# Kernel optimization log

Hardware: AMD Instinct MI355X
Metric: run time of the kernel (lower is better)

Reference implementation:

```python
import jax, jax.numpy as jnp
import numpy as np

HID = 128
OUT = 1
L = 4
N_NODES = 50000
N_EDGES = 600000
NUM_GRAPHS = 256
ATOM_FEATS, ATOM_VOCAB = 9, 64
BOND_FEATS, BOND_VOCAB = 3, 8
BN_EPS = 1e-5


def setup_inputs() -> dict:
    key = jax.random.key(0)
    ks = jax.random.split(key, 16)
    x = jax.random.randint(ks[0], (N_NODES, ATOM_FEATS), 0, ATOM_VOCAB)
    edge_index = jax.random.randint(ks[1], (2, N_EDGES), 0, N_NODES)
    edge_attr = jax.random.randint(ks[2], (N_EDGES, BOND_FEATS), 0, BOND_VOCAB)
    batch = jnp.sort(jax.random.randint(ks[3], (N_NODES,), 0, NUM_GRAPHS))
    s = 0.05
    atom_emb = jax.random.normal(ks[4], (ATOM_FEATS, ATOM_VOCAB, HID), jnp.float32) * s
    bond_emb = jax.random.normal(ks[5], (BOND_FEATS, BOND_VOCAB, HID), jnp.float32) * s
    lin1_w = jax.random.normal(ks[6], (L, HID, HID), jnp.float32) * (1.0 / np.sqrt(HID))
    lin1_b = jnp.zeros((L, HID), jnp.float32)
    lin2_w = jax.random.normal(ks[7], (L, HID, HID), jnp.float32) * (1.0 / np.sqrt(HID))
    lin2_b = jnp.zeros((L, HID), jnp.float32)
    bn_gamma = jnp.ones((L, HID), jnp.float32)
    bn_beta = jnp.zeros((L, HID), jnp.float32)
    bn_mean = jax.random.normal(ks[8], (L, HID), jnp.float32) * 0.1
    bn_var = jax.random.uniform(ks[9], (L, HID), jnp.float32, 0.5, 1.5)
    mlp_w = jax.random.normal(ks[10], (HID, OUT), jnp.float32) * (1.0 / np.sqrt(HID))
    mlp_b = jnp.zeros((OUT,), jnp.float32)
    return dict(x=x, edge_index=edge_index, edge_attr=edge_attr, batch=batch,
                atom_emb=atom_emb, bond_emb=bond_emb,
                lin1_w=lin1_w, lin1_b=lin1_b, lin2_w=lin2_w, lin2_b=lin2_b,
                bn_gamma=bn_gamma, bn_beta=bn_beta, bn_mean=bn_mean, bn_var=bn_var,
                mlp_w=mlp_w, mlp_b=mlp_b)


def _multi_embed(tables, idx):
    # tables: [F, V, H], idx: [N, F] -> sum over F of tables[f][idx[:, f]] -> [N, H]
    return jax.vmap(lambda tab, i: tab[i], in_axes=(0, 1))(tables, idx).sum(0)


def reference(x, edge_index, edge_attr, batch, atom_emb, bond_emb,
              lin1_w, lin1_b, lin2_w, lin2_b, bn_gamma, bn_beta,
              bn_mean, bn_var, mlp_w, mlp_b):
    h = _multi_embed(atom_emb, x)            # [N, H]
    e = _multi_embed(bond_emb, edge_attr)    # [E, H]
    src, dst = edge_index[0], edge_index[1]
    for l in range(L):
        x_res = h
        # GINEConv (eps=0): MLP(x + sum_j ReLU(x_j + e_ji))
        msg = jax.nn.relu(h[src] + e)                          # [E, H]
        agg = jax.ops.segment_sum(msg, dst, num_segments=N_NODES)
        z = h + agg
        z = jax.nn.relu(z @ lin1_w[l] + lin1_b[l]) @ lin2_w[l] + lin2_b[l]
        # BatchNorm (eval: running stats)
        z = (z - bn_mean[l]) * (bn_gamma[l] / jnp.sqrt(bn_var[l] + BN_EPS)) + bn_beta[l]
        h = x_res + jax.nn.relu(z)
        # dropout is identity in eval mode
    sums = jax.ops.segment_sum(h, batch, num_segments=NUM_GRAPHS)
    cnt = jax.ops.segment_sum(jnp.ones((N_NODES, 1), h.dtype), batch, num_segments=NUM_GRAPHS)
    pooled = sums / jnp.maximum(cnt, 1.0)
    return pooled @ mlp_w + mlp_b
```

## Files before the change

### kernel.cpp

```cpp
#include <hip/hip_runtime.h>

#define NNODES 50000
#define NEDGES 600000
#define NGRAPH 256
#define HD     128
#define NLAYER 4
#define NBLK_SCAN 49

typedef __bf16 bf16;
typedef __attribute__((ext_vector_type(2))) __bf16 bf16x2;
typedef __attribute__((ext_vector_type(4))) __bf16 bf16x4;
typedef __attribute__((ext_vector_type(8))) __bf16 bf16x8;
typedef __attribute__((ext_vector_type(4))) float  f32x4;

#define CB_MLPW 0
#define CB_MLPB 128

struct PtrPack { const void* p[12]; };

__device__ __forceinline__ float ldf(const void* p, int i, int flag) {
    return flag ? (float)((const bf16*)p)[i] : ((const float*)p)[i];
}
__device__ __forceinline__ float blo(unsigned u) { return __uint_as_float(u << 16); }
__device__ __forceinline__ float bhi(unsigned u) { return __uint_as_float(u & 0xFFFF0000u); }

__global__ __launch_bounds__(256) void k_prep(PtrPack pk, const int* __restrict__ x,
                                              float* __restrict__ cvt, bf16* __restrict__ wtg,
                                              float* __restrict__ biasf, float* __restrict__ scalef,
                                              float* __restrict__ shiftf, bf16* __restrict__ etab,
                                              bf16* __restrict__ hbuf) {
    const int flag = (((const unsigned*)pk.p[6])[0] != 0x3F800000u);
    int b = blockIdx.x, t = threadIdx.x;
    if (b < 512) {
        int idx = b * 256 + t;
        int mat = idx >> 14, rem = idx & 16383;
        int k = rem >> 7, n = rem & 127;
        const void* src = (mat < 4) ? pk.p[2] : pk.p[4];
        int mi = (mat < 4) ? mat : mat - 4;
        wtg[((size_t)mat << 14) + (n << 7) + k] = (bf16)ldf(src, (mi << 14) + (k << 7) + n, flag);
    } else if (b < 514) {
        int i = (b - 512) * 256 + t;
        biasf[i] = ldf(pk.p[3], i, flag);
        float s = ldf(pk.p[6], i, flag) * rsqrtf(ldf(pk.p[9], i, flag) + 1e-5f);
        scalef[i] = s;
        shiftf[i] = (ldf(pk.p[5], i, flag) - ldf(pk.p[8], i, flag)) * s + ldf(pk.p[7], i, flag);
    } else if (b == 514) {
        if (t < 128)       cvt[CB_MLPW + t] = ldf(pk.p[10], t, flag);
        else if (t == 128) cvt[CB_MLPB] = ldf(pk.p[11], 0, flag);
    } else if (b < 771) {
        int idx = (b - 515) * 256 + t;
        int combo = idx >> 7, ch = idx & 127;
        int c0 = combo & 7, c1 = (combo >> 3) & 7, c2 = combo >> 6;
        float v = ldf(pk.p[1], (c0 << 7) + ch, flag) +
                  ldf(pk.p[1], ((8 + c1) << 7) + ch, flag) +
                  ldf(pk.p[1], ((16 + c2) << 7) + ch, flag);
        etab[idx] = (bf16)v;
    } else {
        int wid = t >> 6, lane = t & 63;
        int n = (b - 771) * 4 + wid;
        if (n >= NNODES) return;
        const int* xr = x + n * 9;
        float ax = 0.f, ay = 0.f;
        if (flag) {
            const char* ae = (const char*)pk.p[0];
#pragma unroll
            for (int f = 0; f < 9; ++f) {
                int v = xr[f];
                unsigned hu = *(const unsigned*)(ae + (((size_t)(f * 64 + v)) << 8) + (lane << 2));
                ax += blo(hu); ay += bhi(hu);
            }
        } else {
            const float* ae = (const float*)pk.p[0];
#pragma unroll
            for (int f = 0; f < 9; ++f) {
                int v = xr[f];
                float2 tv = ((const float2*)(ae + (((size_t)(f * 64 + v)) << 7)))[lane];
                ax += tv.x; ay += tv.y;
            }
        }
        bf16x2 hv; hv[0] = (bf16)ax; hv[1] = (bf16)ay;
        ((bf16x2*)(hbuf + ((size_t)n << 7)))[lane] = hv;
    }
}

__global__ void k_hist(const int* __restrict__ ei, int* __restrict__ deg) {
    int i = blockIdx.x * 256 + threadIdx.x;
    if (i < NEDGES) atomicAdd(&deg[ei[NEDGES + i]], 1);
}

__global__ void k_scan1(const int* __restrict__ deg, int* __restrict__ partials) {
    __shared__ int s[256];
    int t = threadIdx.x, b = blockIdx.x;
    int base = b * 1024 + t * 4;
    int sum = 0;
#pragma unroll
    for (int i = 0; i < 4; ++i) { int idx = base + i; if (idx < NNODES) sum += deg[idx]; }
    s[t] = sum; __syncthreads();
    for (int o = 128; o > 0; o >>= 1) { if (t < o) s[t] += s[t + o]; __syncthreads(); }
    if (t == 0) partials[b] = s[0];
}

__global__ void k_scan3(const int* __restrict__ deg, const int* __restrict__ partials,
                        int* __restrict__ row_start, int* __restrict__ cursor) {
    __shared__ int s[256];
    __shared__ int boff;
    int t = threadIdx.x, b = blockIdx.x;
    if (t < 64) {
        int own = (t < b && t < NBLK_SCAN) ? partials[t] : 0;
#pragma unroll
        for (int o = 32; o > 0; o >>= 1) own += __shfl_xor(own, o);
        if (t == 0) boff = own;
    }
    int base = b * 1024 + t * 4;
    int v[4]; int sum = 0;
#pragma unroll
    for (int i = 0; i < 4; ++i) {
        int idx = base + i;
        v[i] = (idx < NNODES) ? deg[idx] : 0;
        sum += v[i];
    }
    s[t] = sum; __syncthreads();
    for (int o = 1; o < 256; o <<= 1) {
        int add = (t >= o) ? s[t - o] : 0;
        __syncthreads();
        s[t] += add;
        __syncthreads();
    }
    int run = s[t] - sum + boff;
#pragma unroll
    for (int i = 0; i < 4; ++i) {
        int idx = base + i;
        if (idx < NNODES) { row_start[idx] = run; cursor[idx] = run; }
        run += v[i];
    }
    if (b == NBLK_SCAN - 1 && t == 255) row_start[NNODES] = run;
}

__global__ void k_fill(const int* __restrict__ ei, const int* __restrict__ ea,
                       int* __restrict__ cursor, unsigned* __restrict__ payload) {
    int i = blockIdx.x * 256 + threadIdx.x;
    if (i >= NEDGES) return;
    int dst = ei[NEDGES + i];
    int pos = atomicAdd(&cursor[dst], 1);
    unsigned p = (unsigned)ei[i] | ((unsigned)ea[3 * i] << 16) |
                 ((unsigned)ea[3 * i + 1] << 19) | ((unsigned)ea[3 * i + 2] << 22);
    payload[pos] = p;
}

__global__ __launch_bounds__(256) void k_agg(const bf16* __restrict__ hbuf,
                                             const bf16* __restrict__ etab,
                                             const int* __restrict__ row_start,
                                             const unsigned* __restrict__ payload,
                                             bf16* __restrict__ zbuf) {
    const int t = threadIdx.x;
    const int wid = t >> 6, lane = t & 63;
    const int quad = lane >> 4, l16 = lane & 15;
    const int n = blockIdx.x * 4 + wid;
    if (n >= NNODES) return;
    const int beg = row_start[n], end = row_start[n + 1];
    const char* hbp = (const char*)hbuf;
    const char* ebp = (const char*)etab;

    float acc[8];
#pragma unroll
    for (int k = 0; k < 8; ++k) acc[k] = 0.f;

    for (int base = beg; base < end; base += 32) {
        int m = end - base; if (m > 32) m = 32;
        unsigned pv = (base + lane < end) ? payload[base + lane] : 0u;
        for (int j = 0; j < m; j += 16) {
            unsigned pe[4]; uint4 he[4]; uint4 ee[4];
#pragma unroll
            for (int i = 0; i < 4; ++i) {
                int idx = j + i * 4 + quad;
                pe[i] = __shfl(pv, idx < m ? idx : 0);
            }
#pragma unroll
            for (int i = 0; i < 4; ++i) {
                he[i] = *(const uint4*)(hbp + (((size_t)(pe[i] & 0xFFFFu)) << 8) + (l16 << 4));
                ee[i] = *(const uint4*)(ebp + (((size_t)((pe[i] >> 16) & 511u)) << 8) + (l16 << 4));
            }
#pragma unroll
            for (int i = 0; i < 4; ++i) {
                bool ok = (j + i * 4 + quad) < m;
                float m0 = fmaxf(blo(he[i].x) + blo(ee[i].x), 0.f);
                float m1 = fmaxf(bhi(he[i].x) + bhi(ee[i].x), 0.f);
                float m2 = fmaxf(blo(he[i].y) + blo(ee[i].y), 0.f);
                float m3 = fmaxf(bhi(he[i].y) + bhi(ee[i].y), 0.f);
                float m4 = fmaxf(blo(he[i].z) + blo(ee[i].z), 0.f);
                float m5 = fmaxf(bhi(he[i].z) + bhi(ee[i].z), 0.f);
                float m6 = fmaxf(blo(he[i].w) + blo(ee[i].w), 0.f);
                float m7 = fmaxf(bhi(he[i].w) + bhi(ee[i].w), 0.f);
                if (ok) {
                    acc[0] += m0; acc[1] += m1; acc[2] += m2; acc[3] += m3;
                    acc[4] += m4; acc[5] += m5; acc[6] += m6; acc[7] += m7;
                }
            }
        }
    }

#pragma unroll
    for (int k = 0; k < 8; ++k) {
        acc[k] += __shfl_xor(acc[k], 16);
        acc[k] += __shfl_xor(acc[k], 32);
    }
    if (quad == 0) {
        uint4 hn = *(const uint4*)(hbp + ((size_t)n << 8) + (l16 << 4));
        bf16x8 z;
        z[0] = (bf16)(blo(hn.x) + acc[0]); z[1] = (bf16)(bhi(hn.x) + acc[1]);
        z[2] = (bf16)(blo(hn.y) + acc[2]); z[3] = (bf16)(bhi(hn.y) + acc[3]);
        z[4] = (bf16)(blo(hn.z) + acc[4]); z[5] = (bf16)(bhi(hn.z) + acc[5]);
        z[6] = (bf16)(blo(hn.w) + acc[6]); z[7] = (bf16)(bhi(hn.w) + acc[7]);
        *(bf16x8*)(zbuf + ((size_t)n << 7) + (l16 << 3)) = z;
    }
}

__global__ __launch_bounds__(256) void k_update(const bf16* __restrict__ zbuf,
                                                bf16* __restrict__ hbuf,
                                                const bf16* __restrict__ wtg,
                                                const float* __restrict__ biasf,
                                                const float* __restrict__ scalef,
                                                const float* __restrict__ shiftf,
                                                int layer) {
    __shared__ __align__(16) bf16 zs[64 * 128];
    __shared__ __align__(16) bf16 wt[128 * 128];
    const int t = threadIdx.x;
    const int w = t >> 6, lane = t & 63, r16 = lane & 15, q = lane >> 4;
    const int m0 = blockIdx.x * 64;

#pragma unroll
    for (int it = 0; it < 4; ++it) {
        int idx = t + it * 256;
        int r = idx >> 4, c = idx & 15;
        int row = m0 + r;
        bf16x8 v;
        if (row < NNODES) v = *(const bf16x8*)(zbuf + ((size_t)row << 7) + (c << 3));
        else { for (int ii = 0; ii < 8; ++ii) v[ii] = (bf16)0.0f; }
        *(bf16x8*)&zs[(r << 7) + ((c ^ (r & 7)) << 3)] = v;
    }
    {
        const bf16* w1 = wtg + ((size_t)layer << 14);
#pragma unroll
        for (int it = 0; it < 8; ++it) {
            int idx = t + it * 256;
            int r = idx >> 4, c = idx & 15;
            *(bf16x8*)&wt[(r << 7) + ((c ^ (r & 7)) << 3)] =
                *(const bf16x8*)(w1 + (r << 7) + (c << 3));
        }
    }
    __syncthreads();

    f32x4 acc[8];
#pragma unroll
    for (int j = 0; j < 8; ++j) acc[j] = (f32x4){0.f, 0.f, 0.f, 0.f};

    const int sw = r16 & 7;
#pragma unroll
    for (int kc = 0; kc < 4; ++kc) {
        int col = (((kc << 2) + q) ^ sw) << 3;
        bf16x8 a0 = *(const bf16x8*)&zs[((w * 16 + r16) << 7) + col];
        bf16x8 bb[8];
#pragma unroll
        for (int j = 0; j < 8; ++j) bb[j] = *(const bf16x8*)&wt[((j * 16 + r16) << 7) + col];
#pragma unroll
        for (int j = 0; j < 8; ++j)
            acc[j] = __builtin_amdgcn_mfma_f32_16x16x32_bf16(a0, bb[j], acc[j], 0, 0, 0);
    }
    {
        const float* b1 = biasf + (layer << 7);
#pragma unroll
        for (int j = 0; j < 8; ++j) {
            int n = j * 16 + r16;
            float bi = b1[n];
#pragma unroll
            for (int rg = 0; rg < 4; ++rg) {
                int row = w * 16 + q * 4 + rg;
                float v = fmaxf(acc[j][rg] + bi, 0.f);
                zs[(row << 7) + (((n >> 3) ^ (row & 7)) << 3) + (n & 7)] = (bf16)v;
            }
        }
    }
    __syncthreads();
    {
        const bf16* w2 = wtg + ((size_t)(NLAYER + layer) << 14);
#pragma unroll
        for (int it = 0; it < 8; ++it) {
            int idx = t + it * 256;
            int r = idx >> 4, c = idx & 15;
            *(bf16x8*)&wt[(r << 7) + ((c ^ (r & 7)) << 3)] =
                *(const bf16x8*)(w2 + (r << 7) + (c << 3));
        }
    }
    __syncthreads();

#pragma unroll
    for (int j = 0; j < 8; ++j) acc[j] = (f32x4){0.f, 0.f, 0.f, 0.f};

#pragma unroll
    for (int kc = 0; kc < 4; ++kc) {
        int col = (((kc << 2) + q) ^ sw) << 3;
        bf16x8 a0 = *(const bf16x8*)&zs[((w * 16 + r16) << 7) + col];
        bf16x8 bb[8];
#pragma unroll
        for (int j = 0; j < 8; ++j) bb[j] = *(const bf16x8*)&wt[((j * 16 + r16) << 7) + col];
#pragma unroll
        for (int j = 0; j < 8; ++j)
            acc[j] = __builtin_amdgcn_mfma_f32_16x16x32_bf16(a0, bb[j], acc[j], 0, 0, 0);
    }
    {
        const float* sc = scalef + (layer << 7);
        const float* sh = shiftf + (layer << 7);
#pragma unroll
        for (int j = 0; j < 8; ++j) {
            int n = j * 16 + r16;
            float s_ = sc[n], h_ = sh[n];
#pragma unroll
            for (int rg = 0; rg < 4; ++rg) {
                int row = w * 16 + q * 4 + rg;
                float z = acc[j][rg] * s_ + h_;
                zs[(row << 7) + (((n >> 3) ^ (row & 7)) << 3) + (n & 7)] = (bf16)fmaxf(z, 0.f);
            }
        }
    }
    __syncthreads();
#pragma unroll
    for (int it = 0; it < 4; ++it) {
        int c = t + it * 256;
        int row = c >> 4, seg = c & 15;
        int grow = m0 + row;
        if (grow < NNODES) {
            bf16x8 zv = *(const bf16x8*)&zs[(row << 7) + ((seg ^ (row & 7)) << 3)];
            bf16* hp = hbuf + ((size_t)grow << 7) + (seg << 3);
            bf16x8 hv = *(const bf16x8*)hp;
            bf16x8 r;
#pragma unroll
            for (int k = 0; k < 8; ++k) r[k] = (bf16)((float)hv[k] + (float)zv[k]);
            *(bf16x8*)hp = r;
        }
    }
}

__global__ __launch_bounds__(256) void k_pool(const bf16* __restrict__ hbuf,
                                              const int* __restrict__ batch,
                                              const float* __restrict__ cvt,
                                              const unsigned* __restrict__ gam_raw,
                                              void* __restrict__ out) {
    const int flag = (*gam_raw != 0x3F800000u);
    int g = blockIdx.x;
    int t = threadIdx.x, wid = t >> 6, lane = t & 63;
    int lo = 0, hi = NNODES;
    while (lo < hi) { int m = (lo + hi) >> 1; if (batch[m] < g) lo = m + 1; else hi = m; }
    int s = lo;
    hi = NNODES;
    while (lo < hi) { int m = (lo + hi) >> 1; if (batch[m] <= g) lo = m + 1; else hi = m; }
    int e = lo;
    float ax = 0.f, ay = 0.f;
    for (int n = s + wid; n < e; n += 4) {
        unsigned hu = ((const unsigned*)(hbuf + ((size_t)n << 7)))[lane];
        ax += blo(hu);
        ay += bhi(hu);
    }
    __shared__ float red[4][128];
    red[wid][2 * lane] = ax;
    red[wid][2 * lane + 1] = ay;
    __syncthreads();
    __shared__ float fin[128];
    if (t < 128) {
        float sum = red[0][t] + red[1][t] + red[2][t] + red[3][t];
        float cnt = fmaxf((float)(e - s), 1.0f);
        fin[t] = (sum / cnt) * cvt[CB_MLPW + t];
    }
    __syncthreads();
    for (int o = 64; o > 0; o >>= 1) {
        if (t < o) fin[t] += fin[t + o];
        __syncthreads();
    }
    if (t == 0) {
        float r = fin[0] + cvt[CB_MLPB];
        if (flag) ((bf16*)out)[g] = (bf16)r;
        else      ((float*)out)[g] = r;
    }
}

extern "C" void kernel_launch(void* const* d_in, const int* in_sizes, int n_in,
                              void* d_out, int out_size, void* d_ws, size_t ws_size,
                              hipStream_t stream) {
    const int* x     = (const int*)d_in[0];
    const int* ei    = (const int*)d_in[1];
    const int* ea    = (const int*)d_in[2];
    const int* batch = (const int*)d_in[3];

    char* ws = (char*)d_ws;
    size_t o = 0;
    auto alloc = [&](size_t bytes) -> void* {
        void* p = ws + o;
        o = (o + bytes + 255) & ~(size_t)255;
        return p;
    };
    bf16*     hbuf      = (bf16*)alloc((size_t)NNODES * HD * 2);
    bf16*     zbuf      = (bf16*)alloc((size_t)NNODES * HD * 2);
    unsigned* payload   = (unsigned*)alloc((size_t)NEDGES * 4);
    int*      row_start = (int*)alloc((size_t)(NNODES + 1) * 4);
    int*      cursor    = (int*)alloc((size_t)NNODES * 4);
    int*      deg       = (int*)alloc((size_t)NNODES * 4);
    int*      partials  = (int*)alloc(64 * 4);
    bf16*     wtg       = (bf16*)alloc((size_t)8 * 128 * 128 * 2);
    bf16*     etab      = (bf16*)alloc((size_t)512 * 128 * 2);
    float*    cvt       = (float*)alloc((size_t)129 * 4);
    float*    biasf     = (float*)alloc(NLAYER * HD * 4);
    float*    scalef    = (float*)alloc(NLAYER * HD * 4);
    float*    shiftf    = (float*)alloc(NLAYER * HD * 4);

    PtrPack pk;
    for (int i = 0; i < 12; ++i) pk.p[i] = d_in[4 + i];
    const unsigned* gam_raw = (const unsigned*)d_in[10];

    hipMemsetAsync(deg, 0, (size_t)NNODES * 4, stream);
    k_hist<<<(NEDGES + 255) / 256, 256, 0, stream>>>(ei, deg);
    k_scan1<<<NBLK_SCAN, 256, 0, stream>>>(deg, partials);
    k_scan3<<<NBLK_SCAN, 256, 0, stream>>>(deg, partials, row_start, cursor);
    k_fill<<<(NEDGES + 255) / 256, 256, 0, stream>>>(ei, ea, cursor, payload);
    k_prep<<<771 + (NNODES + 3) / 4, 256, 0, stream>>>(pk, x, cvt, wtg, biasf, scalef, shiftf, etab, hbuf);
    for (int l = 0; l < NLAYER; ++l) {
        k_agg<<<(NNODES + 3) / 4, 256, 0, stream>>>(hbuf, etab, row_start, payload, zbuf);
        k_update<<<(NNODES + 63) / 64, 256, 0, stream>>>(zbuf, hbuf, wtg, biasf, scalef, shiftf, l);
    }
    k_pool<<<NGRAPH, 256, 0, stream>>>(hbuf, batch, cvt, gam_raw, d_out);
}
```

Baseline: 383.1 us.

## Fuse edge aggregation into per-layer MLP kernel with ping-pong node buffers

Merges the neighbor aggregation and the MLP/BatchNorm update into one kernel per layer. Each block gathers messages for its 64 nodes directly into shared memory, so the z intermediate never goes through global memory. Node features now alternate between two buffers so the in-place update does not race with other blocks' gathers. The degree histogram is folded into the prep kernel to save a launch. In exchange, each block has only 4 waves doing serial gather loops over 16 nodes each, and there are 4x fewer blocks for the latency-bound gather phase, so latency hiding may suffer.

```diff
diff --git a/kernel.cpp b/kernel.cpp
--- a/kernel.cpp
+++ b/kernel.cpp
@@ -9,13 +9,19 @@
 
 typedef __bf16 bf16;
 typedef __attribute__((ext_vector_type(2))) __bf16 bf16x2;
-typedef __attribute__((ext_vector_type(4))) __bf16 bf16x4;
 typedef __attribute__((ext_vector_type(8))) __bf16 bf16x8;
 typedef __attribute__((ext_vector_type(4))) float  f32x4;
 
 #define CB_MLPW 0
 #define CB_MLPB 128
 
+#define PB_W    512
+#define PB_BN   (PB_W + 2)
+#define PB_MLP  (PB_BN + 1)
+#define PB_ETAB (PB_MLP + 256)
+#define PB_EMB  (PB_ETAB + 12500)
+#define PB_HIST (PB_EMB + 2344)
+
 struct PtrPack { const void* p[12]; };
 
 __device__ __forceinline__ float ldf(const void* p, int i, int flag) {
@@ -25,39 +31,40 @@
 __device__ __forceinline__ float bhi(unsigned u) { return __uint_as_float(u & 0xFFFF0000u); }
 
 __global__ __launch_bounds__(256) void k_prep(PtrPack pk, const int* __restrict__ x,
+                                              const int* __restrict__ ei,
                                               float* __restrict__ cvt, bf16* __restrict__ wtg,
                                               float* __restrict__ biasf, float* __restrict__ scalef,
                                               float* __restrict__ shiftf, bf16* __restrict__ etab,
-                                              bf16* __restrict__ hbuf) {
+                                              bf16* __restrict__ hbuf, int* __restrict__ deg) {
     const int flag = (((const unsigned*)pk.p[6])[0] != 0x3F800000u);
     int b = blockIdx.x, t = threadIdx.x;
-    if (b < 512) {
+    if (b < PB_W) {
         int idx = b * 256 + t;
         int mat = idx >> 14, rem = idx & 16383;
         int k = rem >> 7, n = rem & 127;
         const void* src = (mat < 4) ? pk.p[2] : pk.p[4];
         int mi = (mat < 4) ? mat : mat - 4;
         wtg[((size_t)mat << 14) + (n << 7) + k] = (bf16)ldf(src, (mi << 14) + (k << 7) + n, flag);
-    } else if (b < 514) {
-        int i = (b - 512) * 256 + t;
+    } else if (b < PB_BN) {
+        int i = (b - PB_W) * 256 + t;
         biasf[i] = ldf(pk.p[3], i, flag);
         float s = ldf(pk.p[6], i, flag) * rsqrtf(ldf(pk.p[9], i, flag) + 1e-5f);
         scalef[i] = s;
         shiftf[i] = (ldf(pk.p[5], i, flag) - ldf(pk.p[8], i, flag)) * s + ldf(pk.p[7], i, flag);
-    } else if (b == 514) {
+    } else if (b < PB_MLP) {
         if (t < 128)       cvt[CB_MLPW + t] = ldf(pk.p[10], t, flag);
         else if (t == 128) cvt[CB_MLPB] = ldf(pk.p[11], 0, flag);
-    } else if (b < 771) {
-        int idx = (b - 515) * 256 + t;
+    } else if (b < PB_ETAB) {
+        int idx = (b - PB_MLP) * 256 + t;
         int combo = idx >> 7, ch = idx & 127;
         int c0 = combo & 7, c1 = (combo >> 3) & 7, c2 = combo >> 6;
         float v = ldf(pk.p[1], (c0 << 7) + ch, flag) +
                   ldf(pk.p[1], ((8 + c1) << 7) + ch, flag) +
                   ldf(pk.p[1], ((16 + c2) << 7) + ch, flag);
         etab[idx] = (bf16)v;
-    } else {
+    } else if (b < PB_EMB) {
         int wid = t >> 6, lane = t & 63;
-        int n = (b - 771) * 4 + wid;
+        int n = (b - PB_ETAB) * 4 + wid;
         if (n >= NNODES) return;
         const int* xr = x + n * 9;
         float ax = 0.f, ay = 0.f;
@@ -80,12 +87,10 @@
         }
         bf16x2 hv; hv[0] = (bf16)ax; hv[1] = (bf16)ay;
         ((bf16x2*)(hbuf + ((size_t)n << 7)))[lane] = hv;
-    }
-}
-
-__global__ void k_hist(const int* __restrict__ ei, int* __restrict__ deg) {
-    int i = blockIdx.x * 256 + threadIdx.x;
-    if (i < NEDGES) atomicAdd(&deg[ei[NEDGES + i]], 1);
+    } else {
+        int i = (b - PB_EMB) * 256 + t;
+        if (i < NEDGES) atomicAdd(&deg[ei[NEDGES + i]], 1);
+    }
 }
 
 __global__ void k_scan1(const int* __restrict__ deg, int* __restrict__ partials) {
@@ -147,97 +152,25 @@
     payload[pos] = p;
 }
 
-__global__ __launch_bounds__(256) void k_agg(const bf16* __restrict__ hbuf,
-                                             const bf16* __restrict__ etab,
-                                             const int* __restrict__ row_start,
-                                             const unsigned* __restrict__ payload,
-                                             bf16* __restrict__ zbuf) {
-    const int t = threadIdx.x;
-    const int wid = t >> 6, lane = t & 63;
-    const int quad = lane >> 4, l16 = lane & 15;
-    const int n = blockIdx.x * 4 + wid;
-    if (n >= NNODES) return;
-    const int beg = row_start[n], end = row_start[n + 1];
-    const char* hbp = (const char*)hbuf;
-    const char* ebp = (const char*)etab;
-
-    float acc[8];
-#pragma unroll
-    for (int k = 0; k < 8; ++k) acc[k] = 0.f;
-
-    for (int base = beg; base < end; base += 32) {
-        int m = end - base; if (m > 32) m = 32;
-        unsigned pv = (base + lane < end) ? payload[base + lane] : 0u;
-        for (int j = 0; j < m; j += 16) {
-            unsigned pe[4]; uint4 he[4]; uint4 ee[4];
-#pragma unroll
-            for (int i = 0; i < 4; ++i) {
-                int idx = j + i * 4 + quad;
-                pe[i] = __shfl(pv, idx < m ? idx : 0);
-            }
-#pragma unroll
-            for (int i = 0; i < 4; ++i) {
-                he[i] = *(const uint4*)(hbp + (((size_t)(pe[i] & 0xFFFFu)) << 8) + (l16 << 4));
-                ee[i] = *(const uint4*)(ebp + (((size_t)((pe[i] >> 16) & 511u)) << 8) + (l16 << 4));
-            }
-#pragma unroll
-            for (int i = 0; i < 4; ++i) {
-                bool ok = (j + i * 4 + quad) < m;
-                float m0 = fmaxf(blo(he[i].x) + blo(ee[i].x), 0.f);
-                float m1 = fmaxf(bhi(he[i].x) + bhi(ee[i].x), 0.f);
-                float m2 = fmaxf(blo(he[i].y) + blo(ee[i].y), 0.f);
-                float m3 = fmaxf(bhi(he[i].y) + bhi(ee[i].y), 0.f);
-                float m4 = fmaxf(blo(he[i].z) + blo(ee[i].z), 0.f);
-                float m5 = fmaxf(bhi(he[i].z) + bhi(ee[i].z), 0.f);
-                float m6 = fmaxf(blo(he[i].w) + blo(ee[i].w), 0.f);
-                float m7 = fmaxf(bhi(he[i].w) + bhi(ee[i].w), 0.f);
-                if (ok) {
-                    acc[0] += m0; acc[1] += m1; acc[2] += m2; acc[3] += m3;
-                    acc[4] += m4; acc[5] += m5; acc[6] += m6; acc[7] += m7;
-                }
-            }
-        }
-    }
-
-#pragma unroll
-    for (int k = 0; k < 8; ++k) {
-        acc[k] += __shfl_xor(acc[k], 16);
-        acc[k] += __shfl_xor(acc[k], 32);
-    }
-    if (quad == 0) {
-        uint4 hn = *(const uint4*)(hbp + ((size_t)n << 8) + (l16 << 4));
-        bf16x8 z;
-        z[0] = (bf16)(blo(hn.x) + acc[0]); z[1] = (bf16)(bhi(hn.x) + acc[1]);
-        z[2] = (bf16)(blo(hn.y) + acc[2]); z[3] = (bf16)(bhi(hn.y) + acc[3]);
-        z[4] = (bf16)(blo(hn.z) + acc[4]); z[5] = (bf16)(bhi(hn.z) + acc[5]);
-        z[6] = (bf16)(blo(hn.w) + acc[6]); z[7] = (bf16)(bhi(hn.w) + acc[7]);
-        *(bf16x8*)(zbuf + ((size_t)n << 7) + (l16 << 3)) = z;
-    }
-}
-
-__global__ __launch_bounds__(256) void k_update(const bf16* __restrict__ zbuf,
-                                                bf16* __restrict__ hbuf,
-                                                const bf16* __restrict__ wtg,
-                                                const float* __restrict__ biasf,
-                                                const float* __restrict__ scalef,
-                                                const float* __restrict__ shiftf,
-                                                int layer) {
+__global__ __launch_bounds__(256) void k_layer(const bf16* __restrict__ hin,
+                                               bf16* __restrict__ hout,
+                                               const bf16* __restrict__ etab,
+                                               const int* __restrict__ row_start,
+                                               const unsigned* __restrict__ payload,
+                                               const bf16* __restrict__ wtg,
+                                               const float* __restrict__ biasf,
+                                               const float* __restrict__ scalef,
+                                               const float* __restrict__ shiftf,
+                                               int layer) {
     __shared__ __align__(16) bf16 zs[64 * 128];
     __shared__ __align__(16) bf16 wt[128 * 128];
     const int t = threadIdx.x;
     const int w = t >> 6, lane = t & 63, r16 = lane & 15, q = lane >> 4;
+    const int quad = lane >> 4, l16 = lane & 15;
     const int m0 = blockIdx.x * 64;
-
-#pragma unroll
-    for (int it = 0; it < 4; ++it) {
-        int idx = t + it * 256;
-        int r = idx >> 4, c = idx & 15;
-        int row = m0 + r;
-        bf16x8 v;
-        if (row < NNODES) v = *(const bf16x8*)(zbuf + ((size_t)row << 7) + (c << 3));
-        else { for (int ii = 0; ii < 8; ++ii) v[ii] = (bf16)0.0f; }
-        *(bf16x8*)&zs[(r << 7) + ((c ^ (r & 7)) << 3)] = v;
-    }
+    const char* hbp = (const char*)hin;
+    const char* ebp = (const char*)etab;
+
     {
         const bf16* w1 = wtg + ((size_t)layer << 14);
 #pragma unroll
@@ -246,6 +179,69 @@
             int r = idx >> 4, c = idx & 15;
             *(bf16x8*)&wt[(r << 7) + ((c ^ (r & 7)) << 3)] =
                 *(const bf16x8*)(w1 + (r << 7) + (c << 3));
+        }
+    }
+
+    for (int i = 0; i < 16; ++i) {
+        const int n = m0 + w * 16 + i;
+        const bool active = n < NNODES;
+        int beg = 0, end = 0;
+        if (active) { beg = row_start[n]; end = row_start[n + 1]; }
+        float acc[8];
+#pragma unroll
+        for (int k = 0; k < 8; ++k) acc[k] = 0.f;
+
+        for (int base = beg; base < end; base += 32) {
+            int m = end - base; if (m > 32) m = 32;
+            unsigned pv = (base + lane < end) ? payload[base + lane] : 0u;
+            for (int j = 0; j < m; j += 16) {
+                unsigned pe[4]; uint4 he[4]; uint4 ee[4];
+#pragma unroll
+                for (int ii = 0; ii < 4; ++ii) {
+                    int idx = j + ii * 4 + quad;
+                    pe[ii] = __shfl(pv, idx < m ? idx : 0);
+                }
+#pragma unroll
+                for (int ii = 0; ii < 4; ++ii) {
+                    he[ii] = *(const uint4*)(hbp + (((size_t)(pe[ii] & 0xFFFFu)) << 8) + (l16 << 4));
+                    ee[ii] = *(const uint4*)(ebp + (((size_t)((pe[ii] >> 16) & 511u)) << 8) + (l16 << 4));
+                }
+#pragma unroll
+                for (int ii = 0; ii < 4; ++ii) {
+                    bool ok = (j + ii * 4 + quad) < m;
+                    float m0_ = fmaxf(blo(he[ii].x) + blo(ee[ii].x), 0.f);
+                    float m1_ = fmaxf(bhi(he[ii].x) + bhi(ee[ii].x), 0.f);
+                    float m2_ = fmaxf(blo(he[ii].y) + blo(ee[ii].y), 0.f);
+                    float m3_ = fmaxf(bhi(he[ii].y) + bhi(ee[ii].y), 0.f);
+                    float m4_ = fmaxf(blo(he[ii].z) + blo(ee[ii].z), 0.f);
+                    float m5_ = fmaxf(bhi(he[ii].z) + bhi(ee[ii].z), 0.f);
+                    float m6_ = fmaxf(blo(he[ii].w) + blo(ee[ii].w), 0.f);
+                    float m7_ = fmaxf(bhi(he[ii].w) + bhi(ee[ii].w), 0.f);
+                    if (ok) {
+                        acc[0] += m0_; acc[1] += m1_; acc[2] += m2_; acc[3] += m3_;
+                        acc[4] += m4_; acc[5] += m5_; acc[6] += m6_; acc[7] += m7_;
+                    }
+                }
+            }
+        }
+#pragma unroll
+        for (int k = 0; k < 8; ++k) {
+            acc[k] += __shfl_xor(acc[k], 16);
+            acc[k] += __shfl_xor(acc[k], 32);
+        }
+        if (quad == 0) {
+            bf16x8 z;
+            if (active) {
+                uint4 hn = *(const uint4*)(hbp + ((size_t)n << 8) + (l16 << 4));
+                z[0] = (bf16)(blo(hn.x) + acc[0]); z[1] = (bf16)(bhi(hn.x) + acc[1]);
+                z[2] = (bf16)(blo(hn.y) + acc[2]); z[3] = (bf16)(bhi(hn.y) + acc[3]);
+                z[4] = (bf16)(blo(hn.z) + acc[4]); z[5] = (bf16)(bhi(hn.z) + acc[5]);
+                z[6] = (bf16)(blo(hn.w) + acc[6]); z[7] = (bf16)(bhi(hn.w) + acc[7]);
+            } else {
+                for (int k = 0; k < 8; ++k) z[k] = (bf16)0.0f;
+            }
+            int row = w * 16 + i;
+            *(bf16x8*)&zs[(row << 7) + ((l16 ^ (row & 7)) << 3)] = z;
         }
     }
     __syncthreads();
@@ -330,12 +326,12 @@
         int grow = m0 + row;
         if (grow < NNODES) {
             bf16x8 zv = *(const bf16x8*)&zs[(row << 7) + ((seg ^ (row & 7)) << 3)];
-            bf16* hp = hbuf + ((size_t)grow << 7) + (seg << 3);
-            bf16x8 hv = *(const bf16x8*)hp;
+            const bf16* hip_ = hin + ((size_t)grow << 7) + (seg << 3);
+            bf16x8 hv = *(const bf16x8*)hip_;
             bf16x8 r;
 #pragma unroll
             for (int k = 0; k < 8; ++k) r[k] = (bf16)((float)hv[k] + (float)zv[k]);
-            *(bf16x8*)hp = r;
+            *(bf16x8*)(hout + ((size_t)grow << 7) + (seg << 3)) = r;
         }
     }
 }
@@ -397,8 +393,8 @@
         o = (o + bytes + 255) & ~(size_t)255;
         return p;
     };
-    bf16*     hbuf      = (bf16*)alloc((size_t)NNODES * HD * 2);
-    bf16*     zbuf      = (bf16*)alloc((size_t)NNODES * HD * 2);
+    bf16*     hA        = (bf16*)alloc((size_t)NNODES * HD * 2);
+    bf16*     hB        = (bf16*)alloc((size_t)NNODES * HD * 2);
     unsigned* payload   = (unsigned*)alloc((size_t)NEDGES * 4);
     int*      row_start = (int*)alloc((size_t)(NNODES + 1) * 4);
     int*      cursor    = (int*)alloc((size_t)NNODES * 4);
@@ -416,14 +412,16 @@
     const unsigned* gam_raw = (const unsigned*)d_in[10];
 
     hipMemsetAsync(deg, 0, (size_t)NNODES * 4, stream);
-    k_hist<<<(NEDGES + 255) / 256, 256, 0, stream>>>(ei, deg);
+    k_prep<<<PB_HIST, 256, 0, stream>>>(pk, x, ei, cvt, wtg, biasf, scalef, shiftf, etab, hA, deg);
     k_scan1<<<NBLK_SCAN, 256, 0, stream>>>(deg, partials);
     k_scan3<<<NBLK_SCAN, 256, 0, stream>>>(deg, partials, row_start, cursor);
     k_fill<<<(NEDGES + 255) / 256, 256, 0, stream>>>(ei, ea, cursor, payload);
-    k_prep<<<771 + (NNODES + 3) / 4, 256, 0, stream>>>(pk, x, cvt, wtg, biasf, scalef, shiftf, etab, hbuf);
+    bf16* hin = hA;
+    bf16* hout = hB;
     for (int l = 0; l < NLAYER; ++l) {
-        k_agg<<<(NNODES + 3) / 4, 256, 0, stream>>>(hbuf, etab, row_start, payload, zbuf);
-        k_update<<<(NNODES + 63) / 64, 256, 0, stream>>>(zbuf, hbuf, wtg, biasf, scalef, shiftf, l);
-    }
-    k_pool<<<NGRAPH, 256, 0, stream>>>(hbuf, batch, cvt, gam_raw, d_out);
-}
+        k_layer<<<(NNODES + 63) / 64, 256, 0, stream>>>(hin, hout, etab, row_start, payload,
+                                                        wtg, biasf, scalef, shiftf, l);
+        bf16* tmp = hin; hin = hout; hout = tmp;
+    }
+    k_pool<<<NGRAPH, 256, 0, stream>>>(hin, batch, cvt, gam_raw, d_out);
+}
```

New measurement: 528.9 us. +38.0%, slower.
